# Kernel tuning notes

Hardware: AMD Instinct MI355X
Metric: run time of the kernel (lower is better)

The kernel has to match this reference:

```python
import jax, jax.numpy as jnp
import numpy as np

ALPHA = 0.2  # LeakyReLU negative slope


def setup_inputs() -> dict:
    key = jax.random.key(0)
    k1, k2, k3, k4 = jax.random.split(key, 4)
    B, N, F_IN, F_OUT = 8, 2048, 512, 256
    h = jax.random.normal(k1, (B, N, F_IN), dtype=jnp.float32)
    # torch nn.Linear weights: [out, in]
    W = jax.random.normal(k2, (F_OUT, F_IN), dtype=jnp.float32) * (1.414 / np.sqrt(F_IN))
    a1 = jax.random.normal(k3, (1, F_OUT), dtype=jnp.float32) * (1.414 / np.sqrt(F_OUT))
    a2 = jax.random.normal(k4, (1, F_OUT), dtype=jnp.float32) * (1.414 / np.sqrt(F_OUT))
    return {"h": h, "W": W, "a1": a1, "a2": a2}


def reference(h, W, a1, a2):
    # Wh: [B, N, F_out]
    Wh = jnp.einsum('bnf,of->bno', h, W)
    # additive attention scores
    s1 = jnp.einsum('bno,o->bn', Wh, a1[0])  # [B, N]
    s2 = jnp.einsum('bno,o->bn', Wh, a2[0])  # [B, N]
    e = s1[:, :, None] + s2[:, None, :]       # [B, N, N]
    e = jnp.where(e > 0, e, ALPHA * e)         # LeakyReLU
    attention = jax.nn.softmax(e, axis=2)      # softmax over last dim
    # dropout p=0.0 -> identity
    h_prime = jnp.einsum('bnm,bmo->bno', attention, Wh)
    return jax.nn.elu(h_prime)  # concat=True path
```

## Files before the change

kernel.cpp:

```cpp
#include <hip/hip_runtime.h>

typedef __attribute__((ext_vector_type(8))) _Float16 half8;
typedef __attribute__((ext_vector_type(4))) _Float16 half4;
typedef __attribute__((ext_vector_type(4))) float f32x4;

#define ALPHA 0.2f

__device__ __forceinline__ void gload_lds16(const void* g, void* l) {
  __builtin_amdgcn_global_load_lds((const __attribute__((address_space(1))) unsigned int*)g,
                                   (__attribute__((address_space(3))) unsigned int*)l, 16, 0, 0);
}

__global__ __launch_bounds__(256) void k_convW(const float* __restrict__ W,
                                               _Float16* __restrict__ W16) {
  int idx4 = blockIdx.x * 256 + threadIdx.x;
  int n = idx4 >> 7;
  int q = idx4 & 127;
  float4 v = *reinterpret_cast<const float4*>(W + n * 512 + q * 4);
  half4 hv = {(_Float16)v.x, (_Float16)v.y, (_Float16)v.z, (_Float16)v.w};
  int kp = (q * 4) ^ ((n & 7) << 3);
  *reinterpret_cast<half4*>(W16 + n * 512 + kp) = hv;
}

__global__ __launch_bounds__(256) void k_uvec(const float* __restrict__ W,
                                              const float* __restrict__ a1,
                                              const float* __restrict__ a2,
                                              float* __restrict__ u1,
                                              float* __restrict__ u2) {
  __shared__ float r1[4], r2[4];
  int k = blockIdx.x, t = threadIdx.x;
  float wv = W[t * 512 + k];
  float x1 = wv * a1[t];
  float x2 = wv * a2[t];
#pragma unroll
  for (int off = 32; off >= 1; off >>= 1) {
    x1 += __shfl_xor(x1, off);
    x2 += __shfl_xor(x2, off);
  }
  if ((t & 63) == 0) { r1[t >> 6] = x1; r2[t >> 6] = x2; }
  __syncthreads();
  if (t == 0) {
    u1[k] = r1[0] + r1[1] + r1[2] + r1[3];
    u2[k] = r2[0] + r2[1] + r2[2] + r2[3];
  }
}

__global__ __launch_bounds__(256) void k_smax(const float* __restrict__ s2,
                                              float* __restrict__ smax) {
  __shared__ float red[4];
  int b = blockIdx.x, t = threadIdx.x;
  float m = -1e30f;
  for (int j = t; j < 2048; j += 256) m = fmaxf(m, s2[b * 2048 + j]);
#pragma unroll
  for (int off = 32; off >= 1; off >>= 1) m = fmaxf(m, __shfl_xor(m, off));
  if ((t & 63) == 0) red[t >> 6] = m;
  __syncthreads();
  if (t == 0) smax[b] = fmaxf(fmaxf(red[0], red[1]), fmaxf(red[2], red[3]));
}

__global__ __launch_bounds__(256) void k_gemm_wh(const float* __restrict__ h,
                                                 const _Float16* __restrict__ W16,
                                                 const float* __restrict__ u1,
                                                 const float* __restrict__ u2,
                                                 float* __restrict__ s1o,
                                                 float* __restrict__ s2o,
                                                 _Float16* __restrict__ WhT) {
  __shared__ _Float16 Ab[2][32 * 64];
  __shared__ _Float16 Bb[2][256 * 64];
  const int t = threadIdx.x, lane = t & 63, w = t >> 6;
  const int i0 = blockIdx.x * 32;
  const int b = i0 >> 11, n0 = i0 & 2047;
  const int ar = t >> 3, au = t & 7;
  const float* hrow = h + (size_t)(i0 + ar) * 512 + au * 8;

  f32x4 acc[2][4];
#pragma unroll
  for (int mi = 0; mi < 2; ++mi)
#pragma unroll
    for (int ni = 0; ni < 4; ++ni) acc[mi][ni] = (f32x4){0.f, 0.f, 0.f, 0.f};

  float4 aR0 = *reinterpret_cast<const float4*>(hrow);
  float4 aR1 = *reinterpret_cast<const float4*>(hrow + 4);
#pragma unroll
  for (int q = 0; q < 8; ++q) {
    int idx = (q * 4 + w) * 64 + lane;
    int nn = idx >> 3, uu = idx & 7;
    gload_lds16(W16 + nn * 512 + uu * 8, (char*)&Bb[0][0] + idx * 16);
  }
  float x1 = 0.f, x2 = 0.f;

  for (int kt = 0; kt < 8; ++kt) {
    const int cur = kt & 1;
    {
      half8 av;
      av[0] = (_Float16)aR0.x; av[1] = (_Float16)aR0.y;
      av[2] = (_Float16)aR0.z; av[3] = (_Float16)aR0.w;
      av[4] = (_Float16)aR1.x; av[5] = (_Float16)aR1.y;
      av[6] = (_Float16)aR1.z; av[7] = (_Float16)aR1.w;
      *reinterpret_cast<half8*>((char*)&Ab[cur][0] + ar * 128 + ((au * 16) ^ ((ar & 7) << 4))) = av;
      const float* up1 = u1 + kt * 64 + au * 8;
      const float* up2 = u2 + kt * 64 + au * 8;
      float4 u1a = *reinterpret_cast<const float4*>(up1);
      float4 u1b = *reinterpret_cast<const float4*>(up1 + 4);
      float4 u2a = *reinterpret_cast<const float4*>(up2);
      float4 u2b = *reinterpret_cast<const float4*>(up2 + 4);
      x1 += aR0.x * u1a.x + aR0.y * u1a.y + aR0.z * u1a.z + aR0.w * u1a.w
          + aR1.x * u1b.x + aR1.y * u1b.y + aR1.z * u1b.z + aR1.w * u1b.w;
      x2 += aR0.x * u2a.x + aR0.y * u2a.y + aR0.z * u2a.z + aR0.w * u2a.w
          + aR1.x * u2b.x + aR1.y * u2b.y + aR1.z * u2b.z + aR1.w * u2b.w;
    }
    __syncthreads();
    if (kt < 7) {
      const int k0 = (kt + 1) * 64;
      aR0 = *reinterpret_cast<const float4*>(hrow + k0);
      aR1 = *reinterpret_cast<const float4*>(hrow + k0 + 4);
#pragma unroll
      for (int q = 0; q < 8; ++q) {
        int idx = (q * 4 + w) * 64 + lane;
        int nn = idx >> 3, uu = idx & 7;
        gload_lds16(W16 + nn * 512 + k0 + uu * 8, (char*)&Bb[cur ^ 1][0] + idx * 16);
      }
    }
    const char* Ac = (const char*)&Ab[cur][0];
    const char* Bc = (const char*)&Bb[cur][0];
#pragma unroll
    for (int kk = 0; kk < 2; ++kk) {
      const int jb = (lane >> 4) * 16 + kk * 64;
      half8 afr[2];
#pragma unroll
      for (int mi = 0; mi < 2; ++mi) {
        int rr = (lane & 15) + 16 * mi;
        afr[mi] = *reinterpret_cast<const half8*>(Ac + rr * 128 + (jb ^ ((rr & 7) << 4)));
      }
#pragma unroll
      for (int ni = 0; ni < 4; ++ni) {
        int nn = 64 * w + 16 * ni + (lane & 15);
        half8 bfr = *reinterpret_cast<const half8*>(Bc + nn * 128 + (jb ^ ((nn & 7) << 4)));
#pragma unroll
        for (int mi = 0; mi < 2; ++mi)
          acc[mi][ni] = __builtin_amdgcn_mfma_f32_16x16x32_f16(afr[mi], bfr, acc[mi][ni], 0, 0, 0);
      }
    }
  }
  x1 += __shfl_xor(x1, 1); x1 += __shfl_xor(x1, 2); x1 += __shfl_xor(x1, 4);
  x2 += __shfl_xor(x2, 1); x2 += __shfl_xor(x2, 2); x2 += __shfl_xor(x2, 4);
  if (au == 0) { s1o[i0 + ar] = x1; s2o[i0 + ar] = x2; }
  _Float16* whtb = WhT + (size_t)b * 256 * 2048;
#pragma unroll
  for (int mi = 0; mi < 2; ++mi)
#pragma unroll
    for (int ni = 0; ni < 4; ++ni) {
      int c = 64 * w + 16 * ni + (lane & 15);
      int nb = n0 + 16 * mi + (lane >> 4) * 4;
      int np = nb ^ ((c & 7) << 3);
      f32x4 a = acc[mi][ni];
      half4 hv = {(_Float16)a[0], (_Float16)a[1], (_Float16)a[2], (_Float16)a[3]};
      *reinterpret_cast<half4*>(whtb + (size_t)c * 2048 + np) = hv;
    }
}

__global__ __launch_bounds__(256) void k_attn(const _Float16* __restrict__ WhT,
                                              const float* __restrict__ s1,
                                              const float* __restrict__ s2,
                                              const float* __restrict__ smax,
                                              float* __restrict__ out) {
  __shared__ _Float16 Bb[2][128 * 64];
  const int t = threadIdx.x, lane = t & 63, w = t >> 6;
  const int bid = blockIdx.x;
  const int b = bid & 7;
  const int r = bid >> 3;
  const int i0 = (r & 31) * 64;
  const int c0 = (r >> 5) * 128;
  const _Float16* whtb = WhT + ((size_t)b * 256 + c0) * 2048;
  const float* s2b = s2 + b * 2048;
  const int arow = lane & 15;
  const int grow = i0 + w * 16 + arow;
  float s1v = s1[b * 2048 + grow];
  float mrow = s1v + smax[b];
  mrow = fmaxf(mrow, ALPHA * mrow);
  float dsum = 0.f;
  f32x4 acc[8];
#pragma unroll
  for (int ni = 0; ni < 8; ++ni) acc[ni] = (f32x4){0.f, 0.f, 0.f, 0.f};

#pragma unroll
  for (int q = 0; q < 4; ++q) {
    int idx = (q * 4 + w) * 64 + lane;
    int cl = idx >> 3, uu = idx & 7;
    gload_lds16(whtb + (size_t)cl * 2048 + uu * 8, (char*)&Bb[0][0] + idx * 16);
  }

  for (int jt = 0; jt < 32; ++jt) {
    const int cur = jt & 1;
    __syncthreads();
    if (jt < 31) {
      const int j0n = (jt + 1) * 64;
#pragma unroll
      for (int q = 0; q < 4; ++q) {
        int idx = (q * 4 + w) * 64 + lane;
        int cl = idx >> 3, uu = idx & 7;
        gload_lds16(whtb + (size_t)cl * 2048 + j0n + uu * 8, (char*)&Bb[cur ^ 1][0] + idx * 16);
      }
    }
    const int j0 = jt * 64;
    const char* Bc = (const char*)&Bb[cur][0];
#pragma unroll
    for (int kk = 0; kk < 2; ++kk) {
      const int jl = (lane >> 4) * 8 + kk * 32;
      float4 sA = *reinterpret_cast<const float4*>(s2b + j0 + jl);
      float4 sB = *reinterpret_cast<const float4*>(s2b + j0 + jl + 4);
      half8 afr;
      float e, p;
      e = s1v + sA.x; e = fmaxf(e, ALPHA * e); p = __expf(e - mrow); afr[0] = (_Float16)p; dsum += p;
      e = s1v + sA.y; e = fmaxf(e, ALPHA * e); p = __expf(e - mrow); afr[1] = (_Float16)p; dsum += p;
      e = s1v + sA.z; e = fmaxf(e, ALPHA * e); p = __expf(e - mrow); afr[2] = (_Float16)p; dsum += p;
      e = s1v + sA.w; e = fmaxf(e, ALPHA * e); p = __expf(e - mrow); afr[3] = (_Float16)p; dsum += p;
      e = s1v + sB.x; e = fmaxf(e, ALPHA * e); p = __expf(e - mrow); afr[4] = (_Float16)p; dsum += p;
      e = s1v + sB.y; e = fmaxf(e, ALPHA * e); p = __expf(e - mrow); afr[5] = (_Float16)p; dsum += p;
      e = s1v + sB.z; e = fmaxf(e, ALPHA * e); p = __expf(e - mrow); afr[6] = (_Float16)p; dsum += p;
      e = s1v + sB.w; e = fmaxf(e, ALPHA * e); p = __expf(e - mrow); afr[7] = (_Float16)p; dsum += p;
      const int jb = jl * 2;
#pragma unroll
      for (int ni = 0; ni < 8; ++ni) {
        int cl = 16 * ni + arow;
        half8 bfr = *reinterpret_cast<const half8*>(Bc + cl * 128 + (jb ^ ((cl & 7) << 4)));
        acc[ni] = __builtin_amdgcn_mfma_f32_16x16x32_f16(afr, bfr, acc[ni], 0, 0, 0);
      }
    }
  }
  dsum += __shfl_xor(dsum, 16);
  dsum += __shfl_xor(dsum, 32);
  float inv[4];
#pragma unroll
  for (int reg = 0; reg < 4; ++reg) {
    float d = __shfl(dsum, (lane >> 4) * 4 + reg);
    inv[reg] = 1.f / d;
  }
  const size_t ob = ((size_t)b * 2048 + i0 + w * 16) * 256 + c0;
#pragma unroll
  for (int ni = 0; ni < 8; ++ni) {
    int c = 16 * ni + arow;
#pragma unroll
    for (int reg = 0; reg < 4; ++reg) {
      int rr = (lane >> 4) * 4 + reg;
      float v = acc[ni][reg] * inv[reg];
      v = v > 0.f ? v : (__expf(v) - 1.f);
      out[ob + (size_t)rr * 256 + c] = v;
    }
  }
}

extern "C" void kernel_launch(void* const* d_in, const int* in_sizes, int n_in,
                              void* d_out, int out_size, void* d_ws, size_t ws_size,
                              hipStream_t stream) {
  (void)in_sizes; (void)n_in; (void)out_size; (void)ws_size;
  const float* h = (const float*)d_in[0];
  const float* W = (const float*)d_in[1];
  const float* a1 = (const float*)d_in[2];
  const float* a2 = (const float*)d_in[3];
  float* out = (float*)d_out;
  char* ws = (char*)d_ws;
  _Float16* WhT = (_Float16*)(ws);
  _Float16* W16 = (_Float16*)(ws + 8388608);
  float* u1 = (float*)(ws + 8650752);
  float* u2 = (float*)(ws + 8652800);
  float* s1 = (float*)(ws + 8654848);
  float* s2 = (float*)(ws + 8720384);
  float* smax = (float*)(ws + 8785920);

  hipLaunchKernelGGL(k_convW, dim3(128), dim3(256), 0, stream, W, W16);
  hipLaunchKernelGGL(k_uvec, dim3(512), dim3(256), 0, stream, W, a1, a2, u1, u2);
  hipLaunchKernelGGL(k_gemm_wh, dim3(512), dim3(256), 0, stream, h, W16, u1, u2, s1, s2, WhT);
  hipLaunchKernelGGL(k_smax, dim3(8), dim3(256), 0, stream, s2, smax);
  hipLaunchKernelGGL(k_attn, dim3(512), dim3(256), 0, stream, WhT, s1, s2, smax, out);
}
```

Before: 75.57 us.

## Retile Wh GEMM and attention kernels, use exp2 softmax and MFMA row sums

The Wh GEMM now uses 16-row tiles over twice as many blocks and reads W fragments straight from global memory instead of staging them in LDS, which also drops the W swizzle. The attention kernel halves its column tile to 64 so it launches twice as many blocks. It folds LeakyReLU and the max subtraction into exp2 with a prescaled s2 produced by k_smax. Row sums of the softmax are now computed with an extra MFMA against a ones vector instead of shuffles, and fp16 packing uses cvt_pkrtz. The trade-offs are more redundant recomputation of the exp terms across column blocks and uncached global B loads in the GEMM.

After: 93.28 us. +23.4%, slower.

```diff
diff --git a/kernel.cpp b/kernel.cpp
--- a/kernel.cpp
+++ b/kernel.cpp
@@ -3,23 +3,32 @@
 typedef __attribute__((ext_vector_type(8))) _Float16 half8;
 typedef __attribute__((ext_vector_type(4))) _Float16 half4;
 typedef __attribute__((ext_vector_type(4))) float f32x4;
+#if __has_builtin(__builtin_amdgcn_cvt_pkrtz)
+typedef __attribute__((ext_vector_type(2))) __fp16 fp16x2;
+#endif
 
 #define ALPHA 0.2f
+#define LOG2E 1.44269504f
 
 __device__ __forceinline__ void gload_lds16(const void* g, void* l) {
   __builtin_amdgcn_global_load_lds((const __attribute__((address_space(1))) unsigned int*)g,
                                    (__attribute__((address_space(3))) unsigned int*)l, 16, 0, 0);
 }
 
+__device__ __forceinline__ float fexp2(float x) {
+#if __has_builtin(__builtin_amdgcn_exp2f)
+  return __builtin_amdgcn_exp2f(x);
+#else
+  return __expf(x * 0.69314718f);
+#endif
+}
+
 __global__ __launch_bounds__(256) void k_convW(const float* __restrict__ W,
                                                _Float16* __restrict__ W16) {
-  int idx4 = blockIdx.x * 256 + threadIdx.x;
-  int n = idx4 >> 7;
-  int q = idx4 & 127;
-  float4 v = *reinterpret_cast<const float4*>(W + n * 512 + q * 4);
+  int i = (blockIdx.x * 256 + threadIdx.x) * 4;
+  float4 v = *reinterpret_cast<const float4*>(W + i);
   half4 hv = {(_Float16)v.x, (_Float16)v.y, (_Float16)v.z, (_Float16)v.w};
-  int kp = (q * 4) ^ ((n & 7) << 3);
-  *reinterpret_cast<half4*>(W16 + n * 512 + kp) = hv;
+  *reinterpret_cast<half4*>(W16 + i) = hv;
 }
 
 __global__ __launch_bounds__(256) void k_uvec(const float* __restrict__ W,
@@ -46,11 +55,16 @@
 }
 
 __global__ __launch_bounds__(256) void k_smax(const float* __restrict__ s2,
-                                              float* __restrict__ smax) {
+                                              float* __restrict__ smax,
+                                              float* __restrict__ s2L) {
   __shared__ float red[4];
   int b = blockIdx.x, t = threadIdx.x;
   float m = -1e30f;
-  for (int j = t; j < 2048; j += 256) m = fmaxf(m, s2[b * 2048 + j]);
+  for (int j = t; j < 2048; j += 256) {
+    float v = s2[b * 2048 + j];
+    s2L[b * 2048 + j] = LOG2E * v;
+    m = fmaxf(m, v);
+  }
 #pragma unroll
   for (int off = 32; off >= 1; off >>= 1) m = fmaxf(m, __shfl_xor(m, off));
   if ((t & 63) == 0) red[t >> 6] = m;
@@ -65,127 +79,106 @@
                                                  float* __restrict__ s1o,
                                                  float* __restrict__ s2o,
                                                  _Float16* __restrict__ WhT) {
-  __shared__ _Float16 Ab[2][32 * 64];
-  __shared__ _Float16 Bb[2][256 * 64];
+  __shared__ _Float16 As[2][16 * 64];
   const int t = threadIdx.x, lane = t & 63, w = t >> 6;
-  const int i0 = blockIdx.x * 32;
-  const int b = i0 >> 11, n0 = i0 & 2047;
-  const int ar = t >> 3, au = t & 7;
-  const float* hrow = h + (size_t)(i0 + ar) * 512 + au * 8;
-
-  f32x4 acc[2][4];
-#pragma unroll
-  for (int mi = 0; mi < 2; ++mi)
-#pragma unroll
-    for (int ni = 0; ni < 4; ++ni) acc[mi][ni] = (f32x4){0.f, 0.f, 0.f, 0.f};
-
-  float4 aR0 = *reinterpret_cast<const float4*>(hrow);
-  float4 aR1 = *reinterpret_cast<const float4*>(hrow + 4);
-#pragma unroll
-  for (int q = 0; q < 8; ++q) {
-    int idx = (q * 4 + w) * 64 + lane;
-    int nn = idx >> 3, uu = idx & 7;
-    gload_lds16(W16 + nn * 512 + uu * 8, (char*)&Bb[0][0] + idx * 16);
-  }
+  const int i0 = blockIdx.x * 16;
+  const int b = i0 >> 11;
+  const int arow = lane & 15;
+  const int srow = t >> 4;
+  const int sch = (t & 15) * 4;
+  const float* hrow = h + (size_t)(i0 + srow) * 512 + sch;
+
+  f32x4 acc[4];
+#pragma unroll
+  for (int ni = 0; ni < 4; ++ni) acc[ni] = (f32x4){0.f, 0.f, 0.f, 0.f};
   float x1 = 0.f, x2 = 0.f;
 
+  {
+    float4 aR = *reinterpret_cast<const float4*>(hrow);
+    float4 ua = *reinterpret_cast<const float4*>(u1 + sch);
+    float4 ub = *reinterpret_cast<const float4*>(u2 + sch);
+    x1 += aR.x * ua.x + aR.y * ua.y + aR.z * ua.z + aR.w * ua.w;
+    x2 += aR.x * ub.x + aR.y * ub.y + aR.z * ub.z + aR.w * ub.w;
+    half4 hv = {(_Float16)aR.x, (_Float16)aR.y, (_Float16)aR.z, (_Float16)aR.w};
+    *reinterpret_cast<half4*>((char*)&As[0][0] + srow * 128 + ((sch * 2) ^ ((srow & 7) << 4))) = hv;
+  }
   for (int kt = 0; kt < 8; ++kt) {
-    const int cur = kt & 1;
-    {
-      half8 av;
-      av[0] = (_Float16)aR0.x; av[1] = (_Float16)aR0.y;
-      av[2] = (_Float16)aR0.z; av[3] = (_Float16)aR0.w;
-      av[4] = (_Float16)aR1.x; av[5] = (_Float16)aR1.y;
-      av[6] = (_Float16)aR1.z; av[7] = (_Float16)aR1.w;
-      *reinterpret_cast<half8*>((char*)&Ab[cur][0] + ar * 128 + ((au * 16) ^ ((ar & 7) << 4))) = av;
-      const float* up1 = u1 + kt * 64 + au * 8;
-      const float* up2 = u2 + kt * 64 + au * 8;
-      float4 u1a = *reinterpret_cast<const float4*>(up1);
-      float4 u1b = *reinterpret_cast<const float4*>(up1 + 4);
-      float4 u2a = *reinterpret_cast<const float4*>(up2);
-      float4 u2b = *reinterpret_cast<const float4*>(up2 + 4);
-      x1 += aR0.x * u1a.x + aR0.y * u1a.y + aR0.z * u1a.z + aR0.w * u1a.w
-          + aR1.x * u1b.x + aR1.y * u1b.y + aR1.z * u1b.z + aR1.w * u1b.w;
-      x2 += aR0.x * u2a.x + aR0.y * u2a.y + aR0.z * u2a.z + aR0.w * u2a.w
-          + aR1.x * u2b.x + aR1.y * u2b.y + aR1.z * u2b.z + aR1.w * u2b.w;
-    }
     __syncthreads();
     if (kt < 7) {
       const int k0 = (kt + 1) * 64;
-      aR0 = *reinterpret_cast<const float4*>(hrow + k0);
-      aR1 = *reinterpret_cast<const float4*>(hrow + k0 + 4);
-#pragma unroll
-      for (int q = 0; q < 8; ++q) {
-        int idx = (q * 4 + w) * 64 + lane;
-        int nn = idx >> 3, uu = idx & 7;
-        gload_lds16(W16 + nn * 512 + k0 + uu * 8, (char*)&Bb[cur ^ 1][0] + idx * 16);
-      }
-    }
-    const char* Ac = (const char*)&Ab[cur][0];
-    const char* Bc = (const char*)&Bb[cur][0];
+      float4 aR = *reinterpret_cast<const float4*>(hrow + k0);
+      float4 ua = *reinterpret_cast<const float4*>(u1 + k0 + sch);
+      float4 ub = *reinterpret_cast<const float4*>(u2 + k0 + sch);
+      x1 += aR.x * ua.x + aR.y * ua.y + aR.z * ua.z + aR.w * ua.w;
+      x2 += aR.x * ub.x + aR.y * ub.y + aR.z * ub.z + aR.w * ub.w;
+      half4 hv = {(_Float16)aR.x, (_Float16)aR.y, (_Float16)aR.z, (_Float16)aR.w};
+      *reinterpret_cast<half4*>((char*)&As[(kt + 1) & 1][0] + srow * 128 + ((sch * 2) ^ ((srow & 7) << 4))) = hv;
+    }
+    const char* Ac = (const char*)&As[kt & 1][0];
 #pragma unroll
     for (int kk = 0; kk < 2; ++kk) {
-      const int jb = (lane >> 4) * 16 + kk * 64;
-      half8 afr[2];
-#pragma unroll
-      for (int mi = 0; mi < 2; ++mi) {
-        int rr = (lane & 15) + 16 * mi;
-        afr[mi] = *reinterpret_cast<const half8*>(Ac + rr * 128 + (jb ^ ((rr & 7) << 4)));
-      }
+      const int koff = (lane >> 4) * 16 + kk * 64;
+      half8 afr = *reinterpret_cast<const half8*>(Ac + arow * 128 + (koff ^ ((arow & 7) << 4)));
+      const int kg = kt * 64 + kk * 32 + (lane >> 4) * 8;
 #pragma unroll
       for (int ni = 0; ni < 4; ++ni) {
-        int nn = 64 * w + 16 * ni + (lane & 15);
-        half8 bfr = *reinterpret_cast<const half8*>(Bc + nn * 128 + (jb ^ ((nn & 7) << 4)));
-#pragma unroll
-        for (int mi = 0; mi < 2; ++mi)
-          acc[mi][ni] = __builtin_amdgcn_mfma_f32_16x16x32_f16(afr[mi], bfr, acc[mi][ni], 0, 0, 0);
-      }
-    }
-  }
-  x1 += __shfl_xor(x1, 1); x1 += __shfl_xor(x1, 2); x1 += __shfl_xor(x1, 4);
-  x2 += __shfl_xor(x2, 1); x2 += __shfl_xor(x2, 2); x2 += __shfl_xor(x2, 4);
-  if (au == 0) { s1o[i0 + ar] = x1; s2o[i0 + ar] = x2; }
+        int n = 64 * w + 16 * ni + arow;
+        half8 bfr = *reinterpret_cast<const half8*>(W16 + n * 512 + kg);
+        acc[ni] = __builtin_amdgcn_mfma_f32_16x16x32_f16(afr, bfr, acc[ni], 0, 0, 0);
+      }
+    }
+  }
+  x1 += __shfl_xor(x1, 1); x1 += __shfl_xor(x1, 2); x1 += __shfl_xor(x1, 4); x1 += __shfl_xor(x1, 8);
+  x2 += __shfl_xor(x2, 1); x2 += __shfl_xor(x2, 2); x2 += __shfl_xor(x2, 4); x2 += __shfl_xor(x2, 8);
+  if ((t & 15) == 0) { s1o[i0 + srow] = x1; s2o[i0 + srow] = x2; }
   _Float16* whtb = WhT + (size_t)b * 256 * 2048;
-#pragma unroll
-  for (int mi = 0; mi < 2; ++mi)
-#pragma unroll
-    for (int ni = 0; ni < 4; ++ni) {
-      int c = 64 * w + 16 * ni + (lane & 15);
-      int nb = n0 + 16 * mi + (lane >> 4) * 4;
-      int np = nb ^ ((c & 7) << 3);
-      f32x4 a = acc[mi][ni];
-      half4 hv = {(_Float16)a[0], (_Float16)a[1], (_Float16)a[2], (_Float16)a[3]};
-      *reinterpret_cast<half4*>(whtb + (size_t)c * 2048 + np) = hv;
-    }
+  const int nb = (i0 & 2047) + (lane >> 4) * 4;
+#pragma unroll
+  for (int ni = 0; ni < 4; ++ni) {
+    int c = 64 * w + 16 * ni + arow;
+    int np = nb ^ ((c & 7) << 3);
+    f32x4 a = acc[ni];
+    half4 hv = {(_Float16)a[0], (_Float16)a[1], (_Float16)a[2], (_Float16)a[3]};
+    *reinterpret_cast<half4*>(whtb + (size_t)c * 2048 + np) = hv;
+  }
 }
 
 __global__ __launch_bounds__(256) void k_attn(const _Float16* __restrict__ WhT,
                                               const float* __restrict__ s1,
-                                              const float* __restrict__ s2,
+                                              const float* __restrict__ s2L,
                                               const float* __restrict__ smax,
                                               float* __restrict__ out) {
-  __shared__ _Float16 Bb[2][128 * 64];
+  __shared__ _Float16 Bb[2][64 * 64];
   const int t = threadIdx.x, lane = t & 63, w = t >> 6;
   const int bid = blockIdx.x;
   const int b = bid & 7;
-  const int r = bid >> 3;
-  const int i0 = (r & 31) * 64;
-  const int c0 = (r >> 5) * 128;
+  const int ib = (bid >> 3) & 31;
+  const int cg = bid >> 8;
+  const int i0 = ib * 64, c0 = cg * 64;
   const _Float16* whtb = WhT + ((size_t)b * 256 + c0) * 2048;
-  const float* s2b = s2 + b * 2048;
+  const float* s2Lb = s2L + b * 2048;
   const int arow = lane & 15;
   const int grow = i0 + w * 16 + arow;
-  float s1v = s1[b * 2048 + grow];
-  float mrow = s1v + smax[b];
-  mrow = fmaxf(mrow, ALPHA * mrow);
-  float dsum = 0.f;
-  f32x4 acc[8];
-#pragma unroll
-  for (int ni = 0; ni < 8; ++ni) acc[ni] = (f32x4){0.f, 0.f, 0.f, 0.f};
-
-#pragma unroll
-  for (int q = 0; q < 4; ++q) {
-    int idx = (q * 4 + w) * 64 + lane;
+  const float s1v = s1[b * 2048 + grow];
+  const float sm = smax[b];
+  const float e0 = s1v + sm;
+  const float mrow = fmaxf(e0, ALPHA * e0);
+  const float C1 = LOG2E * (s1v - mrow);
+  const float C2 = fmaf(ALPHA * LOG2E, s1v, -LOG2E * mrow);
+  half8 onesb;
+  {
+    _Float16 ov = (arow == 0) ? (_Float16)1.0f : (_Float16)0.0f;
+#pragma unroll
+    for (int x = 0; x < 8; ++x) onesb[x] = ov;
+  }
+  f32x4 acc[4];
+#pragma unroll
+  for (int ni = 0; ni < 4; ++ni) acc[ni] = (f32x4){0.f, 0.f, 0.f, 0.f};
+  f32x4 accd = (f32x4){0.f, 0.f, 0.f, 0.f};
+
+#pragma unroll
+  for (int q = 0; q < 2; ++q) {
+    int idx = q * 256 + t;
     int cl = idx >> 3, uu = idx & 7;
     gload_lds16(whtb + (size_t)cl * 2048 + uu * 8, (char*)&Bb[0][0] + idx * 16);
   }
@@ -196,8 +189,8 @@
     if (jt < 31) {
       const int j0n = (jt + 1) * 64;
 #pragma unroll
-      for (int q = 0; q < 4; ++q) {
-        int idx = (q * 4 + w) * 64 + lane;
+      for (int q = 0; q < 2; ++q) {
+        int idx = q * 256 + t;
         int cl = idx >> 3, uu = idx & 7;
         gload_lds16(whtb + (size_t)cl * 2048 + j0n + uu * 8, (char*)&Bb[cur ^ 1][0] + idx * 16);
       }
@@ -207,43 +200,52 @@
 #pragma unroll
     for (int kk = 0; kk < 2; ++kk) {
       const int jl = (lane >> 4) * 8 + kk * 32;
-      float4 sA = *reinterpret_cast<const float4*>(s2b + j0 + jl);
-      float4 sB = *reinterpret_cast<const float4*>(s2b + j0 + jl + 4);
+      float4 sA = *reinterpret_cast<const float4*>(s2Lb + j0 + jl);
+      float4 sB = *reinterpret_cast<const float4*>(s2Lb + j0 + jl + 4);
+      float p0 = fexp2(fmaxf(C1 + sA.x, fmaf(ALPHA, sA.x, C2)));
+      float p1 = fexp2(fmaxf(C1 + sA.y, fmaf(ALPHA, sA.y, C2)));
+      float p2 = fexp2(fmaxf(C1 + sA.z, fmaf(ALPHA, sA.z, C2)));
+      float p3 = fexp2(fmaxf(C1 + sA.w, fmaf(ALPHA, sA.w, C2)));
+      float p4 = fexp2(fmaxf(C1 + sB.x, fmaf(ALPHA, sB.x, C2)));
+      float p5 = fexp2(fmaxf(C1 + sB.y, fmaf(ALPHA, sB.y, C2)));
+      float p6 = fexp2(fmaxf(C1 + sB.z, fmaf(ALPHA, sB.z, C2)));
+      float p7 = fexp2(fmaxf(C1 + sB.w, fmaf(ALPHA, sB.w, C2)));
       half8 afr;
-      float e, p;
-      e = s1v + sA.x; e = fmaxf(e, ALPHA * e); p = __expf(e - mrow); afr[0] = (_Float16)p; dsum += p;
-      e = s1v + sA.y; e = fmaxf(e, ALPHA * e); p = __expf(e - mrow); afr[1] = (_Float16)p; dsum += p;
-      e = s1v + sA.z; e = fmaxf(e, ALPHA * e); p = __expf(e - mrow); afr[2] = (_Float16)p; dsum += p;
-      e = s1v + sA.w; e = fmaxf(e, ALPHA * e); p = __expf(e - mrow); afr[3] = (_Float16)p; dsum += p;
-      e = s1v + sB.x; e = fmaxf(e, ALPHA * e); p = __expf(e - mrow); afr[4] = (_Float16)p; dsum += p;
-      e = s1v + sB.y; e = fmaxf(e, ALPHA * e); p = __expf(e - mrow); afr[5] = (_Float16)p; dsum += p;
-      e = s1v + sB.z; e = fmaxf(e, ALPHA * e); p = __expf(e - mrow); afr[6] = (_Float16)p; dsum += p;
-      e = s1v + sB.w; e = fmaxf(e, ALPHA * e); p = __expf(e - mrow); afr[7] = (_Float16)p; dsum += p;
+#if __has_builtin(__builtin_amdgcn_cvt_pkrtz)
+      {
+        fp16x2 q0 = __builtin_amdgcn_cvt_pkrtz(p0, p1);
+        fp16x2 q1 = __builtin_amdgcn_cvt_pkrtz(p2, p3);
+        fp16x2 q2 = __builtin_amdgcn_cvt_pkrtz(p4, p5);
+        fp16x2 q3 = __builtin_amdgcn_cvt_pkrtz(p6, p7);
+        afr[0] = (_Float16)q0[0]; afr[1] = (_Float16)q0[1];
+        afr[2] = (_Float16)q1[0]; afr[3] = (_Float16)q1[1];
+        afr[4] = (_Float16)q2[0]; afr[5] = (_Float16)q2[1];
+        afr[6] = (_Float16)q3[0]; afr[7] = (_Float16)q3[1];
+      }
+#else
+      afr[0] = (_Float16)p0; afr[1] = (_Float16)p1; afr[2] = (_Float16)p2; afr[3] = (_Float16)p3;
+      afr[4] = (_Float16)p4; afr[5] = (_Float16)p5; afr[6] = (_Float16)p6; afr[7] = (_Float16)p7;
+#endif
+      accd = __builtin_amdgcn_mfma_f32_16x16x32_f16(afr, onesb, accd, 0, 0, 0);
       const int jb = jl * 2;
 #pragma unroll
-      for (int ni = 0; ni < 8; ++ni) {
+      for (int ni = 0; ni < 4; ++ni) {
         int cl = 16 * ni + arow;
         half8 bfr = *reinterpret_cast<const half8*>(Bc + cl * 128 + (jb ^ ((cl & 7) << 4)));
         acc[ni] = __builtin_amdgcn_mfma_f32_16x16x32_f16(afr, bfr, acc[ni], 0, 0, 0);
       }
     }
   }
-  dsum += __shfl_xor(dsum, 16);
-  dsum += __shfl_xor(dsum, 32);
-  float inv[4];
+  const size_t ob = ((size_t)b * 2048 + i0 + w * 16) * 256 + c0;
 #pragma unroll
   for (int reg = 0; reg < 4; ++reg) {
-    float d = __shfl(dsum, (lane >> 4) * 4 + reg);
-    inv[reg] = 1.f / d;
-  }
-  const size_t ob = ((size_t)b * 2048 + i0 + w * 16) * 256 + c0;
-#pragma unroll
-  for (int ni = 0; ni < 8; ++ni) {
-    int c = 16 * ni + arow;
-#pragma unroll
-    for (int reg = 0; reg < 4; ++reg) {
-      int rr = (lane >> 4) * 4 + reg;
-      float v = acc[ni][reg] * inv[reg];
+    float dv = __shfl(accd[reg], lane & 48);
+    float inv = 1.0f / dv;
+    int rr = (lane >> 4) * 4 + reg;
+#pragma unroll
+    for (int ni = 0; ni < 4; ++ni) {
+      int c = 16 * ni + arow;
+      float v = acc[ni][reg] * inv;
       v = v > 0.f ? v : (__expf(v) - 1.f);
       out[ob + (size_t)rr * 256 + c] = v;
     }
@@ -267,10 +269,11 @@
   float* s1 = (float*)(ws + 8654848);
   float* s2 = (float*)(ws + 8720384);
   float* smax = (float*)(ws + 8785920);
+  float* s2L = (float*)(ws + 8785952);
 
   hipLaunchKernelGGL(k_convW, dim3(128), dim3(256), 0, stream, W, W16);
   hipLaunchKernelGGL(k_uvec, dim3(512), dim3(256), 0, stream, W, a1, a2, u1, u2);
-  hipLaunchKernelGGL(k_gemm_wh, dim3(512), dim3(256), 0, stream, h, W16, u1, u2, s1, s2, WhT);
-  hipLaunchKernelGGL(k_smax, dim3(8), dim3(256), 0, stream, s2, smax);
-  hipLaunchKernelGGL(k_attn, dim3(512), dim3(256), 0, stream, WhT, s1, s2, smax, out);
-}
+  hipLaunchKernelGGL(k_gemm_wh, dim3(1024), dim3(256), 0, stream, h, W16, u1, u2, s1, s2, WhT);
+  hipLaunchKernelGGL(k_smax, dim3(8), dim3(256), 0, stream, s2, smax, s2L);
+  hipLaunchKernelGGL(k_attn, dim3(1024), dim3(256), 0, stream, WhT, s1, s2L, smax, out);
+}
```

## Restructure attention kernel with 32x32 MFMA, per-wave column slices, fused row max

Applied to the files above, without the earlier changes.

The attention kernel is rewritten so each block handles 32 rows and all 256 columns, with each wave owning a 64-column slice streamed into its own double-buffered LDS region through vmcnt-based waits instead of block barriers. It uses 32x32x16 MFMAs, stages log2-scaled s2 in LDS, and computes the softmax max in-kernel, which removes the separate smax launch. The exponentials use exp2 with precomputed constants and round-toward-zero packed fp16 conversion. k_uvec is reorganised to 8 blocks that loop over outputs. The intent is fewer launches, fewer barriers, less ALU work per score and higher MFMA efficiency. The trade-off is more LDS per block, and every block now recomputes the max over s2.

Result: slower. 85.08 us (+12.6%).

```diff
diff --git a/kernel.cpp b/kernel.cpp
--- a/kernel.cpp
+++ b/kernel.cpp
@@ -3,12 +3,25 @@
 typedef __attribute__((ext_vector_type(8))) _Float16 half8;
 typedef __attribute__((ext_vector_type(4))) _Float16 half4;
 typedef __attribute__((ext_vector_type(4))) float f32x4;
+typedef __attribute__((ext_vector_type(16))) float f32x16;
+#if __has_builtin(__builtin_amdgcn_cvt_pkrtz)
+typedef __attribute__((ext_vector_type(2))) __fp16 fp16x2;
+#endif
 
 #define ALPHA 0.2f
+#define LOG2E 1.44269504f
 
 __device__ __forceinline__ void gload_lds16(const void* g, void* l) {
   __builtin_amdgcn_global_load_lds((const __attribute__((address_space(1))) unsigned int*)g,
                                    (__attribute__((address_space(3))) unsigned int*)l, 16, 0, 0);
+}
+
+__device__ __forceinline__ float fexp2(float x) {
+#if __has_builtin(__builtin_amdgcn_exp2f)
+  return __builtin_amdgcn_exp2f(x);
+#else
+  return exp2f(x);
+#endif
 }
 
 __global__ __launch_bounds__(256) void k_convW(const float* __restrict__ W,
@@ -27,35 +40,22 @@
                                               const float* __restrict__ a2,
                                               float* __restrict__ u1,
                                               float* __restrict__ u2) {
-  __shared__ float r1[4], r2[4];
-  int k = blockIdx.x, t = threadIdx.x;
-  float wv = W[t * 512 + k];
-  float x1 = wv * a1[t];
-  float x2 = wv * a2[t];
-#pragma unroll
-  for (int off = 32; off >= 1; off >>= 1) {
-    x1 += __shfl_xor(x1, off);
-    x2 += __shfl_xor(x2, off);
-  }
-  if ((t & 63) == 0) { r1[t >> 6] = x1; r2[t >> 6] = x2; }
+  __shared__ float p1[4][64], p2[4][64];
+  int t = threadIdx.x;
+  int l = t & 63, g = t >> 6;
+  int k = blockIdx.x * 64 + l;
+  float x1 = 0.f, x2 = 0.f;
+  for (int o = g * 64; o < g * 64 + 64; ++o) {
+    float wv = W[o * 512 + k];
+    x1 += wv * a1[o];
+    x2 += wv * a2[o];
+  }
+  p1[g][l] = x1; p2[g][l] = x2;
   __syncthreads();
-  if (t == 0) {
-    u1[k] = r1[0] + r1[1] + r1[2] + r1[3];
-    u2[k] = r2[0] + r2[1] + r2[2] + r2[3];
-  }
-}
-
-__global__ __launch_bounds__(256) void k_smax(const float* __restrict__ s2,
-                                              float* __restrict__ smax) {
-  __shared__ float red[4];
-  int b = blockIdx.x, t = threadIdx.x;
-  float m = -1e30f;
-  for (int j = t; j < 2048; j += 256) m = fmaxf(m, s2[b * 2048 + j]);
-#pragma unroll
-  for (int off = 32; off >= 1; off >>= 1) m = fmaxf(m, __shfl_xor(m, off));
-  if ((t & 63) == 0) red[t >> 6] = m;
-  __syncthreads();
-  if (t == 0) smax[b] = fmaxf(fmaxf(red[0], red[1]), fmaxf(red[2], red[3]));
+  if (g == 0) {
+    u1[k] = p1[0][l] + p1[1][l] + p1[2][l] + p1[3][l];
+    u2[k] = p2[0][l] + p2[1][l] + p2[2][l] + p2[3][l];
+  }
 }
 
 __global__ __launch_bounds__(256) void k_gemm_wh(const float* __restrict__ h,
@@ -162,92 +162,141 @@
 __global__ __launch_bounds__(256) void k_attn(const _Float16* __restrict__ WhT,
                                               const float* __restrict__ s1,
                                               const float* __restrict__ s2,
-                                              const float* __restrict__ smax,
                                               float* __restrict__ out) {
-  __shared__ _Float16 Bb[2][128 * 64];
-  const int t = threadIdx.x, lane = t & 63, w = t >> 6;
-  const int bid = blockIdx.x;
-  const int b = bid & 7;
-  const int r = bid >> 3;
-  const int i0 = (r & 31) * 64;
-  const int c0 = (r >> 5) * 128;
-  const _Float16* whtb = WhT + ((size_t)b * 256 + c0) * 2048;
-  const float* s2b = s2 + b * 2048;
-  const int arow = lane & 15;
-  const int grow = i0 + w * 16 + arow;
-  float s1v = s1[b * 2048 + grow];
-  float mrow = s1v + smax[b];
-  mrow = fmaxf(mrow, ALPHA * mrow);
+  __shared__ _Float16 Bsl[4][2][64 * 64];
+  __shared__ float s2s[2048];
+  __shared__ float red[4];
+  const int t = threadIdx.x, lane = t & 63, cg = t >> 6;
+  const int b = blockIdx.x & 7;
+  const int i0 = (blockIdx.x >> 3) * 32;
+  const _Float16* whtb = WhT + ((size_t)b * 256 + cg * 64) * 2048;
+
+  float4 sa0 = *reinterpret_cast<const float4*>(s2 + b * 2048 + t * 8);
+  float4 sb0 = *reinterpret_cast<const float4*>(s2 + b * 2048 + t * 8 + 4);
+  float m0 = fmaxf(fmaxf(fmaxf(sa0.x, sa0.y), fmaxf(sa0.z, sa0.w)),
+                   fmaxf(fmaxf(sb0.x, sb0.y), fmaxf(sb0.z, sb0.w)));
+  *reinterpret_cast<float4*>(&s2s[t * 8]) =
+      make_float4(sa0.x * LOG2E, sa0.y * LOG2E, sa0.z * LOG2E, sa0.w * LOG2E);
+  *reinterpret_cast<float4*>(&s2s[t * 8 + 4]) =
+      make_float4(sb0.x * LOG2E, sb0.y * LOG2E, sb0.z * LOG2E, sb0.w * LOG2E);
+#pragma unroll
+  for (int off = 32; off >= 1; off >>= 1) m0 = fmaxf(m0, __shfl_xor(m0, off));
+  if (lane == 0) red[cg] = m0;
+  const float s1v = s1[b * 2048 + i0 + (lane & 31)];
+  __syncthreads();
+  const float smaxL = fmaxf(fmaxf(red[0], red[1]), fmaxf(red[2], red[3])) * LOG2E;
+  const float s1L = LOG2E * s1v;
+  const float e0L = s1L + smaxL;
+  const float mrowL = fmaxf(e0L, ALPHA * e0L);
+  const float C1 = s1L - mrowL;
+  const float C2 = fmaf(ALPHA, s1L, -mrowL);
+
+  f32x16 acc0 = (f32x16)(0.f), acc1 = (f32x16)(0.f);
   float dsum = 0.f;
-  f32x4 acc[8];
-#pragma unroll
-  for (int ni = 0; ni < 8; ++ni) acc[ni] = (f32x4){0.f, 0.f, 0.f, 0.f};
-
-#pragma unroll
-  for (int q = 0; q < 4; ++q) {
-    int idx = (q * 4 + w) * 64 + lane;
-    int cl = idx >> 3, uu = idx & 7;
-    gload_lds16(whtb + (size_t)cl * 2048 + uu * 8, (char*)&Bb[0][0] + idx * 16);
-  }
-
-  for (int jt = 0; jt < 32; ++jt) {
-    const int cur = jt & 1;
-    __syncthreads();
-    if (jt < 31) {
-      const int j0n = (jt + 1) * 64;
-#pragma unroll
-      for (int q = 0; q < 4; ++q) {
-        int idx = (q * 4 + w) * 64 + lane;
-        int cl = idx >> 3, uu = idx & 7;
-        gload_lds16(whtb + (size_t)cl * 2048 + j0n + uu * 8, (char*)&Bb[cur ^ 1][0] + idx * 16);
-      }
-    }
-    const int j0 = jt * 64;
-    const char* Bc = (const char*)&Bb[cur][0];
-#pragma unroll
-    for (int kk = 0; kk < 2; ++kk) {
-      const int jl = (lane >> 4) * 8 + kk * 32;
-      float4 sA = *reinterpret_cast<const float4*>(s2b + j0 + jl);
-      float4 sB = *reinterpret_cast<const float4*>(s2b + j0 + jl + 4);
-      half8 afr;
-      float e, p;
-      e = s1v + sA.x; e = fmaxf(e, ALPHA * e); p = __expf(e - mrow); afr[0] = (_Float16)p; dsum += p;
-      e = s1v + sA.y; e = fmaxf(e, ALPHA * e); p = __expf(e - mrow); afr[1] = (_Float16)p; dsum += p;
-      e = s1v + sA.z; e = fmaxf(e, ALPHA * e); p = __expf(e - mrow); afr[2] = (_Float16)p; dsum += p;
-      e = s1v + sA.w; e = fmaxf(e, ALPHA * e); p = __expf(e - mrow); afr[3] = (_Float16)p; dsum += p;
-      e = s1v + sB.x; e = fmaxf(e, ALPHA * e); p = __expf(e - mrow); afr[4] = (_Float16)p; dsum += p;
-      e = s1v + sB.y; e = fmaxf(e, ALPHA * e); p = __expf(e - mrow); afr[5] = (_Float16)p; dsum += p;
-      e = s1v + sB.z; e = fmaxf(e, ALPHA * e); p = __expf(e - mrow); afr[6] = (_Float16)p; dsum += p;
-      e = s1v + sB.w; e = fmaxf(e, ALPHA * e); p = __expf(e - mrow); afr[7] = (_Float16)p; dsum += p;
-      const int jb = jl * 2;
-#pragma unroll
-      for (int ni = 0; ni < 8; ++ni) {
-        int cl = 16 * ni + arow;
-        half8 bfr = *reinterpret_cast<const half8*>(Bc + cl * 128 + (jb ^ ((cl & 7) << 4)));
-        acc[ni] = __builtin_amdgcn_mfma_f32_16x16x32_f16(afr, bfr, acc[ni], 0, 0, 0);
-      }
-    }
-  }
-  dsum += __shfl_xor(dsum, 16);
+
+  char* const dst0 = (char*)&Bsl[cg][0][0];
+  char* const dst1 = (char*)&Bsl[cg][1][0];
+#define ISSUE_B(JT, DST)                                                              \
+  {                                                                                   \
+    const _Float16* src_ = whtb + (JT) * 64;                                          \
+    _Pragma("unroll") for (int q = 0; q < 8; ++q) {                                   \
+      int idx_ = q * 64 + lane;                                                       \
+      gload_lds16(src_ + (size_t)(idx_ >> 3) * 2048 + (idx_ & 7) * 8, (DST) + idx_ * 16); \
+    }                                                                                 \
+  }
+
+#define COMPUTE_T(JT, SRC)                                                            \
+  {                                                                                   \
+    const char* Bc_ = (SRC);                                                          \
+    const int jw_ = (lane >> 5);                                                      \
+    _Pragma("unroll") for (int ks = 0; ks < 4; ++ks) {                                \
+      const int jo_ = (JT) * 64 + ks * 16 + jw_ * 8;                                  \
+      float4 va_ = *reinterpret_cast<const float4*>(&s2s[jo_]);                       \
+      float4 vb_ = *reinterpret_cast<const float4*>(&s2s[jo_ + 4]);                   \
+      float p0 = fexp2(fmaxf(C1 + va_.x, fmaf(ALPHA, va_.x, C2)));                    \
+      float p1 = fexp2(fmaxf(C1 + va_.y, fmaf(ALPHA, va_.y, C2)));                    \
+      float p2 = fexp2(fmaxf(C1 + va_.z, fmaf(ALPHA, va_.z, C2)));                    \
+      float p3 = fexp2(fmaxf(C1 + va_.w, fmaf(ALPHA, va_.w, C2)));                    \
+      float p4 = fexp2(fmaxf(C1 + vb_.x, fmaf(ALPHA, vb_.x, C2)));                    \
+      float p5 = fexp2(fmaxf(C1 + vb_.y, fmaf(ALPHA, vb_.y, C2)));                    \
+      float p6 = fexp2(fmaxf(C1 + vb_.z, fmaf(ALPHA, vb_.z, C2)));                    \
+      float p7 = fexp2(fmaxf(C1 + vb_.w, fmaf(ALPHA, vb_.w, C2)));                    \
+      dsum += ((p0 + p1) + (p2 + p3)) + ((p4 + p5) + (p6 + p7));                      \
+      half8 ph;                                                                       \
+      PACK8(ph, p0, p1, p2, p3, p4, p5, p6, p7);                                      \
+      const int jb_ = ks * 32 + jw_ * 16;                                             \
+      {                                                                               \
+        int cl_ = (lane & 31);                                                        \
+        half8 bfr = *reinterpret_cast<const half8*>(Bc_ + cl_ * 128 + (jb_ ^ ((cl_ & 7) << 4))); \
+        acc0 = __builtin_amdgcn_mfma_f32_32x32x16_f16(ph, bfr, acc0, 0, 0, 0);        \
+      }                                                                               \
+      {                                                                               \
+        int cl_ = 32 + (lane & 31);                                                   \
+        half8 bfr = *reinterpret_cast<const half8*>(Bc_ + cl_ * 128 + (jb_ ^ ((cl_ & 7) << 4))); \
+        acc1 = __builtin_amdgcn_mfma_f32_32x32x16_f16(ph, bfr, acc1, 0, 0, 0);        \
+      }                                                                               \
+    }                                                                                 \
+  }
+
+#if __has_builtin(__builtin_amdgcn_cvt_pkrtz)
+#define PACK8(PH, a0, a1, a2, a3, a4, a5, a6, a7)                  \
+  {                                                                \
+    fp16x2 q0_ = __builtin_amdgcn_cvt_pkrtz(a0, a1);               \
+    fp16x2 q1_ = __builtin_amdgcn_cvt_pkrtz(a2, a3);               \
+    fp16x2 q2_ = __builtin_amdgcn_cvt_pkrtz(a4, a5);               \
+    fp16x2 q3_ = __builtin_amdgcn_cvt_pkrtz(a6, a7);               \
+    PH[0] = (_Float16)q0_[0]; PH[1] = (_Float16)q0_[1];            \
+    PH[2] = (_Float16)q1_[0]; PH[3] = (_Float16)q1_[1];            \
+    PH[4] = (_Float16)q2_[0]; PH[5] = (_Float16)q2_[1];            \
+    PH[6] = (_Float16)q3_[0]; PH[7] = (_Float16)q3_[1];            \
+  }
+#else
+#define PACK8(PH, a0, a1, a2, a3, a4, a5, a6, a7)                  \
+  {                                                                \
+    PH[0] = (_Float16)a0; PH[1] = (_Float16)a1;                    \
+    PH[2] = (_Float16)a2; PH[3] = (_Float16)a3;                    \
+    PH[4] = (_Float16)a4; PH[5] = (_Float16)a5;                    \
+    PH[6] = (_Float16)a6; PH[7] = (_Float16)a7;                    \
+  }
+#endif
+
+  ISSUE_B(0, dst0);
+  ISSUE_B(1, dst1);
+#pragma unroll 1
+  for (int jt = 0; jt < 30; ++jt) {
+    asm volatile("s_waitcnt vmcnt(8)" ::: "memory");
+    char* sl = (jt & 1) ? dst1 : dst0;
+    COMPUTE_T(jt, sl);
+    __builtin_amdgcn_sched_barrier(0);
+    ISSUE_B(jt + 2, sl);
+  }
+  asm volatile("s_waitcnt vmcnt(8)" ::: "memory");
+  COMPUTE_T(30, dst0);
+  asm volatile("s_waitcnt vmcnt(0)" ::: "memory");
+  COMPUTE_T(31, dst1);
+
   dsum += __shfl_xor(dsum, 32);
-  float inv[4];
-#pragma unroll
-  for (int reg = 0; reg < 4; ++reg) {
-    float d = __shfl(dsum, (lane >> 4) * 4 + reg);
-    inv[reg] = 1.f / d;
-  }
-  const size_t ob = ((size_t)b * 2048 + i0 + w * 16) * 256 + c0;
-#pragma unroll
-  for (int ni = 0; ni < 8; ++ni) {
-    int c = 16 * ni + arow;
-#pragma unroll
-    for (int reg = 0; reg < 4; ++reg) {
-      int rr = (lane >> 4) * 4 + reg;
-      float v = acc[ni][reg] * inv[reg];
-      v = v > 0.f ? v : (__expf(v) - 1.f);
-      out[ob + (size_t)rr * 256 + c] = v;
-    }
-  }
+  float inv[16];
+#pragma unroll
+  for (int reg = 0; reg < 16; ++reg) {
+    int rr = (reg & 3) + 8 * (reg >> 2) + 4 * (lane >> 5);
+    inv[reg] = 1.0f / __shfl(dsum, rr);
+  }
+  const int col = cg * 64 + (lane & 31);
+#pragma unroll
+  for (int reg = 0; reg < 16; ++reg) {
+    int rr = (reg & 3) + 8 * (reg >> 2) + 4 * (lane >> 5);
+    size_t obase = ((size_t)b * 2048 + i0 + rr) * 256 + col;
+    float v0 = acc0[reg] * inv[reg];
+    v0 = v0 > 0.f ? v0 : (fexp2(v0 * LOG2E) - 1.f);
+    out[obase] = v0;
+    float v1 = acc1[reg] * inv[reg];
+    v1 = v1 > 0.f ? v1 : (fexp2(v1 * LOG2E) - 1.f);
+    out[obase + 32] = v1;
+  }
+#undef ISSUE_B
+#undef COMPUTE_T
+#undef PACK8
 }
 
 extern "C" void kernel_launch(void* const* d_in, const int* in_sizes, int n_in,
@@ -266,11 +315,9 @@
   float* u2 = (float*)(ws + 8652800);
   float* s1 = (float*)(ws + 8654848);
   float* s2 = (float*)(ws + 8720384);
-  float* smax = (float*)(ws + 8785920);
 
   hipLaunchKernelGGL(k_convW, dim3(128), dim3(256), 0, stream, W, W16);
-  hipLaunchKernelGGL(k_uvec, dim3(512), dim3(256), 0, stream, W, a1, a2, u1, u2);
+  hipLaunchKernelGGL(k_uvec, dim3(8), dim3(256), 0, stream, W, a1, a2, u1, u2);
   hipLaunchKernelGGL(k_gemm_wh, dim3(512), dim3(256), 0, stream, h, W16, u1, u2, s1, s2, WhT);
-  hipLaunchKernelGGL(k_smax, dim3(8), dim3(256), 0, stream, s2, smax);
-  hipLaunchKernelGGL(k_attn, dim3(512), dim3(256), 0, stream, WhT, s1, s2, smax, out);
-}
+  hipLaunchKernelGGL(k_attn, dim3(512), dim3(256), 0, stream, WhT, s1, s2, out);
+}
```
